# Performance work log

Measured on AMD Instinct MI355X. Metric: run time of the kernel, lower is better.

The kernel has to match this reference:

```python
import jax, jax.numpy as jnp
import numpy as np

B, T, D = 64, 512, 1536   # batch, time, enc_size (2*768)
H = 30                    # z_rnn_size
L_SUP, R_SUP = -0.1, 1.1  # HardKuma stretched support
EPS = 1e-5


def setup_inputs() -> dict:
    key = jax.random.key(0)
    ks = jax.random.split(key, 12)
    s = 0.02
    return {
        "x": jax.random.normal(ks[0], (B, T, D), dtype=jnp.float32),
        "u": jax.random.uniform(ks[1], (B, T, 1), dtype=jnp.float32),
        # LSTMCell(enc_size + 1 -> H), torch gate order [i, f, g, o]
        "Wih": jax.random.normal(ks[2], (4 * H, D + 1), dtype=jnp.float32) * s,
        "Whh": jax.random.normal(ks[3], (4 * H, H), dtype=jnp.float32) * s,
        "bih": jax.random.normal(ks[4], (4 * H,), dtype=jnp.float32) * s,
        "bhh": jax.random.normal(ks[5], (4 * H,), dtype=jnp.float32) * s,
        # KumaGate: Linear(D + H -> 1) + Softplus for a and b
        "Wa": jax.random.normal(ks[6], (1, D + H), dtype=jnp.float32) * s,
        "ba": jax.random.normal(ks[7], (1,), dtype=jnp.float32) * s,
        "Wb": jax.random.normal(ks[8], (1, D + H), dtype=jnp.float32) * s,
        "bb": jax.random.normal(ks[9], (1,), dtype=jnp.float32) * s,
    }


def reference(x, u, Wih, Whh, bih, bhh, Wa, ba, Wb, bb):
    # x: [B, T, D], u: [B, T, 1] uniform reparam noise
    hseq = jnp.swapaxes(x, 0, 1)               # [T, B, D]
    useq = jnp.swapaxes(u, 0, 1)               # [T, B, 1]
    batch = x.shape[0]

    def step(carry, inp):
        hx, cx = carry                          # [B, H] each
        h_t, u_t = inp                          # [B, D], [B, 1]
        feat = jnp.concatenate([h_t, hx], axis=-1)          # [B, D+H]
        a = jnp.clip(jax.nn.softplus(feat @ Wa.T + ba), 1e-6, 100.0)
        b = jnp.clip(jax.nn.softplus(feat @ Wb.T + bb), 1e-6, 100.0)
        # HardKuma reparameterized sample (training branch)
        uu = jnp.clip(u_t, EPS, 1.0 - EPS)
        s = (1.0 - (1.0 - uu) ** (1.0 / b)) ** (1.0 / a)     # Kuma icdf
        t = s * (R_SUP - L_SUP) + L_SUP                      # stretch
        z_t = jnp.clip(t, 0.0, 1.0)                          # hard rectify, [B, 1]
        # LSTMCell update (torch gate order i, f, g, o)
        rnn_in = jnp.concatenate([h_t, z_t], axis=-1)        # [B, D+1]
        gates = rnn_in @ Wih.T + bih + hx @ Whh.T + bhh      # [B, 4H]
        i, f, g, o = jnp.split(gates, 4, axis=-1)
        c_new = jax.nn.sigmoid(f) * cx + jax.nn.sigmoid(i) * jnp.tanh(g)
        h_new = jax.nn.sigmoid(o) * jnp.tanh(c_new)
        return (h_new, c_new), z_t

    init = (jnp.zeros((batch, H), x.dtype), jnp.zeros((batch, H), x.dtype))
    _, zs = jax.lax.scan(step, init, (hseq, useq))           # zs: [T, B, 1]
    return jnp.swapaxes(zs[..., 0], 0, 1)                    # [B, T]
```

## Files before the change

kernel.cpp:

```cpp
#include <hip/hip_runtime.h>
#include <math.h>

#define Bb 64
#define Tt 512
#define Dd 1536
#define Hh 30
#define NC 128
#define Mm (Bb*Tt)
#define KSTEPS 48

typedef unsigned short u16;
typedef __attribute__((ext_vector_type(8))) short short8v;
typedef __attribute__((ext_vector_type(4))) float f32x4;

__device__ __forceinline__ float rcpf_(float x) { return __builtin_amdgcn_rcpf(x); }
__device__ __forceinline__ float sigmoidf_(float x) {
    return rcpf_(1.f + __expf(-x));
}
__device__ __forceinline__ float tanhf_fast(float x) {
    float e = __expf(2.f * x);
    return fmaf(-2.f, rcpf_(e + 1.f), 1.f);
}
__device__ __forceinline__ float softplus_(float x) {
    return fmaxf(x, 0.f) + __logf(1.f + __expf(-fabsf(x)));
}
__device__ __forceinline__ float rl_f(float v, int lane) {
    return __uint_as_float(__builtin_amdgcn_readlane(__float_as_uint(v), lane));
}

#define QPERM(src, CTRL) \
    __uint_as_float((unsigned)__builtin_amdgcn_mov_dpp((int)__float_as_uint(src), CTRL, 0xF, 0xF, false))

#define GLOAD_LDS16(gp, lp) \
    __builtin_amdgcn_global_load_lds((const __attribute__((address_space(1))) void*)(const void*)(gp), \
                                     (__attribute__((address_space(3))) void*)(void*)(lp), 16, 0, 0)

__device__ __forceinline__ f32x4 mm_bf16(short8v a, short8v b, f32x4 c) {
    return __builtin_amdgcn_mfma_f32_16x16x32_bf16(a, b, c, 0, 0, 0);
}

union U4S8 { unsigned int u[4]; short8v s; };

__device__ __forceinline__ void cvt_split(const float4 a, const float4 b,
                                          short8v& hi, short8v& lo) {
    float x[8] = {a.x, a.y, a.z, a.w, b.x, b.y, b.z, b.w};
    U4S8 H, L;
#pragma unroll
    for (int i = 0; i < 4; i++) {
        unsigned int u0 = __float_as_uint(x[2 * i]);
        unsigned int u1 = __float_as_uint(x[2 * i + 1]);
        unsigned int h0 = u0 & 0xffff0000u;
        unsigned int h1 = u1 & 0xffff0000u;
        H.u[i] = (u0 >> 16) | h1;
        float l0 = x[2 * i]     - __uint_as_float(h0);
        float l1 = x[2 * i + 1] - __uint_as_float(h1);
        L.u[i] = (__float_as_uint(l0) >> 16) | (__float_as_uint(l1) & 0xffff0000u);
    }
    hi = H.s;
    lo = L.s;
}

__global__ __launch_bounds__(256) void pack_w(const float* __restrict__ Wih,
                                              const float* __restrict__ Wa,
                                              const float* __restrict__ Wb,
                                              u16* __restrict__ Wbh,
                                              u16* __restrict__ Wbl) {
    const int k = blockIdx.x * 256 + threadIdx.x;
    const int c = blockIdx.y;
    float v = 0.f;
    if (c < 120)       v = Wih[c * (Dd + 1) + k];
    else if (c == 120) v = Wa[k];
    else if (c == 121) v = Wb[k];
    unsigned int u = __float_as_uint(v);
    unsigned int h = u & 0xffff0000u;
    float lo = v - __uint_as_float(h);
    Wbh[(size_t)c * Dd + k] = (u16)(u >> 16);
    Wbl[(size_t)c * Dd + k] = (u16)(__float_as_uint(lo) >> 16);
}

__global__ __launch_bounds__(64) void pack_s3(const float* __restrict__ Wih,
                                              const float* __restrict__ Whh,
                                              const float* __restrict__ Wa,
                                              const float* __restrict__ Wb,
                                              float* __restrict__ WS3) {
    const int l = threadIdx.x;
    const int q = l >> 2, g = l & 3;
    float v0[32], v1[32];
#pragma unroll
    for (int j = 0; j < 32; j++) { v0[j] = 0.f; v1[j] = 0.f; }
    {
        int c0 = g * 30 + q;
        for (int j = 0; j < 30; j++) v0[j] = Whh[c0 * Hh + j];
        v0[30] = Wih[c0 * (Dd + 1) + Dd];
    }
    if (q < 14) {
        int c1 = g * 30 + 16 + q;
        for (int j = 0; j < 30; j++) v1[j] = Whh[c1 * Hh + j];
        v1[30] = Wih[c1 * (Dd + 1) + Dd];
    } else if (l == 56) {
        for (int j = 0; j < 30; j++) v1[j] = Wa[Dd + j];
    } else if (l == 60) {
        for (int j = 0; j < 30; j++) v1[j] = Wb[Dd + j];
    }
    float* dst = WS3 + (size_t)l * 64;
    for (int j = 0; j < 32; j++) { dst[j] = v0[j]; dst[32 + j] = v1[j]; }
}

__global__ __launch_bounds__(256, 2) void gemm_k(const float* __restrict__ X,
                                                 const u16* __restrict__ Wbh,
                                                 const u16* __restrict__ Wbl,
                                                 const float* __restrict__ bih,
                                                 const float* __restrict__ bhh,
                                                 const float* __restrict__ ba,
                                                 const float* __restrict__ bbp,
                                                 float* __restrict__ GX) {
    const int t    = threadIdx.x;
    const int lane = t & 63;
    const int wid  = t >> 6;
    const int wrow = wid >> 1;
    const int wcol = wid & 1;
    const int m0   = blockIdx.x * 64 + wrow * 32;
    const int n0   = wcol * 64;
    const int lr   = lane & 15;
    const int lk   = lane >> 4;

    const float* xa0 = X + (size_t)(m0 + lr) * Dd + lk * 8;
    const float* xa1 = xa0 + (size_t)16 * Dd;
    const u16*   pbh = Wbh + (size_t)(n0 + lr) * Dd + lk * 8;
    const u16*   pbl = Wbl + (size_t)(n0 + lr) * Dd + lk * 8;

    f32x4 acc[2][4];
#pragma unroll
    for (int nt = 0; nt < 4; nt++) {
        int c = n0 + nt * 16 + lr;
        float bv = (c < 120) ? (bih[c] + bhh[c])
                 : (c == 120) ? ba[0]
                 : (c == 121) ? bbp[0] : 0.f;
        f32x4 v = {bv, bv, bv, bv};
        acc[0][nt] = v;
        acc[1][nt] = v;
    }

#define LOADA(ra, ks) do {                                        \
        ra[0] = *(const float4*)(xa0 + (ks) * 32);                \
        ra[1] = *(const float4*)(xa0 + (ks) * 32 + 4);            \
        ra[2] = *(const float4*)(xa1 + (ks) * 32);                \
        ra[3] = *(const float4*)(xa1 + (ks) * 32 + 4);            \
    } while (0)

#define LOADB(bh, bl, ks) do {                                               \
        _Pragma("unroll")                                                    \
        for (int nt = 0; nt < 4; nt++) {                                     \
            bh[nt] = *(const short8v*)(pbh + (size_t)nt * 16 * Dd + (ks) * 32); \
            bl[nt] = *(const short8v*)(pbl + (size_t)nt * 16 * Dd + (ks) * 32); \
        }                                                                    \
    } while (0)

#define STEP(ra, bh, bl) do {                                     \
        short8v ah0, al0, ah1, al1;                               \
        cvt_split(ra[0], ra[1], ah0, al0);                        \
        cvt_split(ra[2], ra[3], ah1, al1);                        \
        _Pragma("unroll")                                         \
        for (int nt = 0; nt < 4; nt++)                            \
            acc[0][nt] = mm_bf16(ah0, bh[nt], acc[0][nt]);        \
        _Pragma("unroll")                                         \
        for (int nt = 0; nt < 4; nt++)                            \
            acc[1][nt] = mm_bf16(ah1, bh[nt], acc[1][nt]);        \
        _Pragma("unroll")                                         \
        for (int nt = 0; nt < 4; nt++)                            \
            acc[0][nt] = mm_bf16(al0, bh[nt], acc[0][nt]);        \
        _Pragma("unroll")                                         \
        for (int nt = 0; nt < 4; nt++)                            \
            acc[1][nt] = mm_bf16(al1, bh[nt], acc[1][nt]);        \
        _Pragma("unroll")                                         \
        for (int nt = 0; nt < 4; nt++)                            \
            acc[0][nt] = mm_bf16(ah0, bl[nt], acc[0][nt]);        \
        _Pragma("unroll")                                         \
        for (int nt = 0; nt < 4; nt++)                            \
            acc[1][nt] = mm_bf16(ah1, bl[nt], acc[1][nt]);        \
    } while (0)

    float4  ra0[4], ra1[4];
    short8v bh0[4], bl0[4], bh1[4], bl1[4];

    LOADA(ra0, 0);
    LOADB(bh0, bl0, 0);
    int ks = 0;
    for (; ks < KSTEPS - 2; ks += 2) {
        LOADA(ra1, ks + 1);
        LOADB(bh1, bl1, ks + 1);
        STEP(ra0, bh0, bl0);
        LOADA(ra0, ks + 2);
        LOADB(bh0, bl0, ks + 2);
        STEP(ra1, bh1, bl1);
    }
    LOADA(ra1, KSTEPS - 1);
    LOADB(bh1, bl1, KSTEPS - 1);
    STEP(ra0, bh0, bl0);
    STEP(ra1, bh1, bl1);

#undef LOADA
#undef LOADB
#undef STEP

#pragma unroll
    for (int mt = 0; mt < 2; mt++)
#pragma unroll
        for (int nt = 0; nt < 4; nt++) {
            float* dst = GX + (size_t)(m0 + mt * 16 + lk * 4) * NC + n0 + nt * 16 + lr;
#pragma unroll
            for (int r = 0; r < 4; r++)
                dst[(size_t)r * NC] = acc[mt][nt][r];
        }
}

#define PIN16(A, B) asm volatile("" \
    : "+v"(A[B+0]), "+v"(A[B+1]), "+v"(A[B+2]),  "+v"(A[B+3]),  "+v"(A[B+4]),  "+v"(A[B+5]),  "+v"(A[B+6]),  "+v"(A[B+7]), \
      "+v"(A[B+8]), "+v"(A[B+9]), "+v"(A[B+10]), "+v"(A[B+11]), "+v"(A[B+12]), "+v"(A[B+13]), "+v"(A[B+14]), "+v"(A[B+15]))

__global__
__attribute__((amdgpu_flat_work_group_size(64, 64)))
__attribute__((amdgpu_waves_per_eu(1)))
void scan_k(const float* __restrict__ u,
            const float* __restrict__ gx,
            const float* __restrict__ WS3,
            float* __restrict__ out) {
    __shared__ float lus[Tt];
    __shared__ float zbuf[Tt];
    __shared__ float gxs[2][32][NC];
    const int b = blockIdx.x;
    const int l = threadIdx.x;
    const int q = l >> 2, g = l & 3;

    for (int k = l; k < Tt; k += 64) {
        float uu = u[b * Tt + k];
        uu = fminf(fmaxf(uu, 1e-5f), 1.f - 1e-5f);
        lus[k] = __logf(1.f - uu);
    }
    __syncthreads();

    float wv0[32], wv1[32];
    {
        const float* wp = WS3 + (size_t)l * 64;
#pragma unroll
        for (int j = 0; j < 8; j++) {
            float4 a4 = ((const float4*)wp)[j];
            float4 b4 = ((const float4*)(wp + 32))[j];
            wv0[4 * j + 0] = a4.x; wv0[4 * j + 1] = a4.y;
            wv0[4 * j + 2] = a4.z; wv0[4 * j + 3] = a4.w;
            wv1[4 * j + 0] = b4.x; wv1[4 * j + 1] = b4.y;
            wv1[4 * j + 2] = b4.z; wv1[4 * j + 3] = b4.w;
        }
    }

    const int c0 = g * 30 + q;
    const int c1 = (q < 14) ? (g * 30 + 16 + q) : ((l == 56) ? 120 : (l == 60) ? 121 : 124);
    const float* gxb0 = gx + (size_t)b * Tt * NC;

    const float mge = (g == 2) ? 2.f : -1.f;

    float hs[Hh];
#pragma unroll
    for (int k = 0; k < Hh; k++) hs[k] = 0.f;
    float cst0 = 0.f, cst1 = 0.f;

#pragma unroll
    for (int j = 0; j < 16; j++)
        GLOAD_LDS16(gxb0 + j * 256 + l * 4, &gxs[0][0][0] + j * 256);
    asm volatile("s_waitcnt vmcnt(0)" ::: "memory");
    float A0 = gxs[0][0][c0], B0 = gxs[0][0][c1], L0 = lus[0];

    for (int c = 0; c < Tt / 32; c++) {
        if (c < Tt / 32 - 1) {
            const float* gch = gxb0 + (size_t)(c + 1) * 32 * NC;
            float* lch = &gxs[(c + 1) & 1][0][0];
#pragma unroll
            for (int j = 0; j < 16; j++)
                GLOAD_LDS16(gch + j * 256 + l * 4, lch + j * 256);
        }
#pragma unroll 1
        for (int s = 0; s < 32; s++) {
            const int t = c * 32 + s;
            PIN16(wv0, 0); PIN16(wv0, 16);
            PIN16(wv1, 0); PIN16(wv1, 16);

            float A1 = 0.f, B1 = 0.f, L1 = 0.f;
            if (t + 1 < Tt) {
                if (s < 31) {
                    A1 = gxs[c & 1][s + 1][c0];
                    B1 = gxs[c & 1][s + 1][c1];
                } else {
                    asm volatile("s_waitcnt vmcnt(0)" ::: "memory");
                    A1 = gxs[(c + 1) & 1][0][c0];
                    B1 = gxs[(c + 1) & 1][0][c1];
                }
                L1 = lus[t + 1];
            }

            float d10 = B0, d11 = 0.f, d12 = 0.f, d13 = 0.f;
#pragma unroll
            for (int k = 0; k < 28; k += 4) {
                d10 = fmaf(wv1[k], hs[k], d10);         d11 = fmaf(wv1[k + 1], hs[k + 1], d11);
                d12 = fmaf(wv1[k + 2], hs[k + 2], d12); d13 = fmaf(wv1[k + 3], hs[k + 3], d13);
            }
            d10 = fmaf(wv1[28], hs[28], d10); d11 = fmaf(wv1[29], hs[29], d11);
            float dot1 = (d10 + d12) + (d11 + d13);

            const float av = rl_f(dot1, 56);
            const float bv = rl_f(dot1, 60);
            float a  = fminf(fmaxf(softplus_(av), 1e-6f), 100.f);
            float bk = fminf(fmaxf(softplus_(bv), 1e-6f), 100.f);
            float lu = L0;
            float p = __expf(lu * rcpf_(bk));
            float inner = 1.f - p;
            float sK = (inner <= 0.f) ? 0.f : __expf(__logf(inner) * rcpf_(a));
            float z = fminf(fmaxf(fmaf(1.2f, sK, -0.1f), 0.f), 1.f);

            float d00 = A0, d01 = 0.f, d02 = 0.f, d03 = 0.f;
#pragma unroll
            for (int k = 0; k < 28; k += 4) {
                d00 = fmaf(wv0[k], hs[k], d00);         d01 = fmaf(wv0[k + 1], hs[k + 1], d01);
                d02 = fmaf(wv0[k + 2], hs[k + 2], d02); d03 = fmaf(wv0[k + 3], hs[k + 3], d03);
            }
            d00 = fmaf(wv0[28], hs[28], d00); d01 = fmaf(wv0[29], hs[29], d01);
            float dot0 = (d00 + d02) + (d01 + d03);

            float acc0 = fmaf(z, wv0[30], dot0);
            float acc1 = fmaf(z, wv1[30], dot1);

            float e0 = __expf(acc0 * mge);
            float e1 = __expf(acc1 * mge);
            float r0 = rcpf_(1.f + e0);
            float r1 = rcpf_(1.f + e1);
            float val0 = (g == 2) ? fmaf(-2.f, r0, 1.f) : r0;
            float val1 = (g == 2) ? fmaf(-2.f, r1, 1.f) : r1;

            float vf0 = QPERM(val0, 0x55), vg0 = QPERM(val0, 0xAA), vo0 = QPERM(val0, 0xFF);
            float vf1 = QPERM(val1, 0x55), vg1 = QPERM(val1, 0xAA), vo1 = QPERM(val1, 0xFF);

            float cn0 = fmaf(vf0, cst0, val0 * vg0);
            float hn0 = vo0 * tanhf_fast(cn0);
            cst0 = cn0;
            float cn1 = fmaf(vf1, cst1, val1 * vg1);
            float hn1 = vo1 * tanhf_fast(cn1);
            cst1 = cn1;

#pragma unroll
            for (int k = 0; k < 16; k++) hs[k] = rl_f(hn0, 4 * k);
#pragma unroll
            for (int k = 16; k < Hh; k++) hs[k] = rl_f(hn1, 4 * (k - 16));

            if (l == 0) zbuf[t] = z;
            A0 = A1; B0 = B1; L0 = L1;
        }
    }
    __syncthreads();
    for (int k = l; k < Tt; k += 64) out[b * Tt + k] = zbuf[k];
}

extern "C" void kernel_launch(void* const* d_in, const int* in_sizes, int n_in,
                              void* d_out, int out_size, void* d_ws, size_t ws_size,
                              hipStream_t stream) {
    const float* x   = (const float*)d_in[0];
    const float* u   = (const float*)d_in[1];
    const float* Wih = (const float*)d_in[2];
    const float* Whh = (const float*)d_in[3];
    const float* bih = (const float*)d_in[4];
    const float* bhh = (const float*)d_in[5];
    const float* Wa  = (const float*)d_in[6];
    const float* ba  = (const float*)d_in[7];
    const float* Wb  = (const float*)d_in[8];
    const float* bbp = (const float*)d_in[9];
    float* out = (float*)d_out;

    char* wsb = (char*)d_ws;
    u16*   Wbh = (u16*)(wsb);
    u16*   Wbl = (u16*)(wsb + 393216);
    float* WS3 = (float*)(wsb + 786432);
    float* GX  = (float*)(wsb + 802816);

    pack_w<<<dim3(Dd / 256, NC), 256, 0, stream>>>(Wih, Wa, Wb, Wbh, Wbl);
    pack_s3<<<1, 64, 0, stream>>>(Wih, Whh, Wa, Wb, WS3);
    gemm_k<<<Mm / 64, 256, 0, stream>>>(x, Wbh, Wbl, bih, bhh, ba, bbp, GX);
    scan_k<<<Bb, 64, 0, stream>>>(u, GX, WS3, out);
}
```

Before: 649.5 us.

## Fuse pack, GEMM and scan into one cooperative kernel with grid syncs

Merges the weight packing, input-projection GEMM and recurrent scan into a single cooperative megakernel of 256 blocks, separated by grid-wide syncs, to remove three kernel-launch boundaries. Each block now does two GEMM tiles, and the scan runs with 256-thread blocks where only 64 threads work. The cost is a serialised scan phase that still sits on 64 blocks, lower occupancy in the GEMM phase (launch bounds 256,1), and grid-sync overhead. The old separate kernels remain as a fallback if the cooperative launch fails.

```diff
diff --git a/kernel.cpp b/kernel.cpp
--- a/kernel.cpp
+++ b/kernel.cpp
@@ -1,5 +1,8 @@
 #include <hip/hip_runtime.h>
+#include <hip/hip_cooperative_groups.h>
 #include <math.h>
+
+namespace cg = cooperative_groups;
 
 #define Bb 64
 #define Tt 512
@@ -60,30 +63,38 @@
     lo = L.s;
 }
 
-__global__ __launch_bounds__(256) void pack_w(const float* __restrict__ Wih,
-                                              const float* __restrict__ Wa,
-                                              const float* __restrict__ Wb,
-                                              u16* __restrict__ Wbh,
-                                              u16* __restrict__ Wbl) {
-    const int k = blockIdx.x * 256 + threadIdx.x;
-    const int c = blockIdx.y;
-    float v = 0.f;
-    if (c < 120)       v = Wih[c * (Dd + 1) + k];
-    else if (c == 120) v = Wa[k];
-    else if (c == 121) v = Wb[k];
-    unsigned int u = __float_as_uint(v);
-    unsigned int h = u & 0xffff0000u;
-    float lo = v - __uint_as_float(h);
-    Wbh[(size_t)c * Dd + k] = (u16)(u >> 16);
-    Wbl[(size_t)c * Dd + k] = (u16)(__float_as_uint(lo) >> 16);
-}
-
-__global__ __launch_bounds__(64) void pack_s3(const float* __restrict__ Wih,
-                                              const float* __restrict__ Whh,
-                                              const float* __restrict__ Wa,
-                                              const float* __restrict__ Wb,
-                                              float* __restrict__ WS3) {
-    const int l = threadIdx.x;
+#define PIN16(A, B) asm volatile("" \
+    : "+v"(A[B+0]), "+v"(A[B+1]), "+v"(A[B+2]),  "+v"(A[B+3]),  "+v"(A[B+4]),  "+v"(A[B+5]),  "+v"(A[B+6]),  "+v"(A[B+7]), \
+      "+v"(A[B+8]), "+v"(A[B+9]), "+v"(A[B+10]), "+v"(A[B+11]), "+v"(A[B+12]), "+v"(A[B+13]), "+v"(A[B+14]), "+v"(A[B+15]))
+
+
+__device__ __forceinline__ void pack_w_body(int i0, int stride,
+                                            const float* __restrict__ Wih,
+                                            const float* __restrict__ Wa,
+                                            const float* __restrict__ Wb,
+                                            u16* __restrict__ Wbh,
+                                            u16* __restrict__ Wbl) {
+    for (int i = i0; i < NC * Dd; i += stride) {
+        int c = i / Dd;
+        int k = i - c * Dd;
+        float v = 0.f;
+        if (c < 120)       v = Wih[c * (Dd + 1) + k];
+        else if (c == 120) v = Wa[k];
+        else if (c == 121) v = Wb[k];
+        unsigned int u = __float_as_uint(v);
+        unsigned int h = u & 0xffff0000u;
+        float lo = v - __uint_as_float(h);
+        Wbh[i] = (u16)(u >> 16);
+        Wbl[i] = (u16)(__float_as_uint(lo) >> 16);
+    }
+}
+
+__device__ __forceinline__ void pack_s3_body(int l,
+                                             const float* __restrict__ Wih,
+                                             const float* __restrict__ Whh,
+                                             const float* __restrict__ Wa,
+                                             const float* __restrict__ Wb,
+                                             float* __restrict__ WS3) {
     const int q = l >> 2, g = l & 3;
     float v0[32], v1[32];
 #pragma unroll
@@ -106,20 +117,20 @@
     for (int j = 0; j < 32; j++) { dst[j] = v0[j]; dst[32 + j] = v1[j]; }
 }
 
-__global__ __launch_bounds__(256, 2) void gemm_k(const float* __restrict__ X,
-                                                 const u16* __restrict__ Wbh,
-                                                 const u16* __restrict__ Wbl,
-                                                 const float* __restrict__ bih,
-                                                 const float* __restrict__ bhh,
-                                                 const float* __restrict__ ba,
-                                                 const float* __restrict__ bbp,
-                                                 float* __restrict__ GX) {
-    const int t    = threadIdx.x;
+__device__ void gemm_tile(int tileIdx, int t,
+                          const float* __restrict__ X,
+                          const u16* __restrict__ Wbh,
+                          const u16* __restrict__ Wbl,
+                          const float* __restrict__ bih,
+                          const float* __restrict__ bhh,
+                          const float* __restrict__ ba,
+                          const float* __restrict__ bbp,
+                          float* __restrict__ GX) {
     const int lane = t & 63;
     const int wid  = t >> 6;
     const int wrow = wid >> 1;
     const int wcol = wid & 1;
-    const int m0   = blockIdx.x * 64 + wrow * 32;
+    const int m0   = tileIdx * 64 + wrow * 32;
     const int n0   = wcol * 64;
     const int lr   = lane & 15;
     const int lk   = lane >> 4;
@@ -214,148 +225,207 @@
         }
 }
 
-#define PIN16(A, B) asm volatile("" \
-    : "+v"(A[B+0]), "+v"(A[B+1]), "+v"(A[B+2]),  "+v"(A[B+3]),  "+v"(A[B+4]),  "+v"(A[B+5]),  "+v"(A[B+6]),  "+v"(A[B+7]), \
-      "+v"(A[B+8]), "+v"(A[B+9]), "+v"(A[B+10]), "+v"(A[B+11]), "+v"(A[B+12]), "+v"(A[B+13]), "+v"(A[B+14]), "+v"(A[B+15]))
-
-__global__
-__attribute__((amdgpu_flat_work_group_size(64, 64)))
-__attribute__((amdgpu_waves_per_eu(1)))
-void scan_k(const float* __restrict__ u,
-            const float* __restrict__ gx,
-            const float* __restrict__ WS3,
-            float* __restrict__ out) {
+__device__ void scan_body(int b, int tid,
+                          const float* __restrict__ u,
+                          const float* __restrict__ gx,
+                          const float* __restrict__ WS3,
+                          float* __restrict__ out) {
     __shared__ float lus[Tt];
     __shared__ float zbuf[Tt];
     __shared__ float gxs[2][32][NC];
-    const int b = blockIdx.x;
-    const int l = threadIdx.x;
-    const int q = l >> 2, g = l & 3;
-
-    for (int k = l; k < Tt; k += 64) {
-        float uu = u[b * Tt + k];
-        uu = fminf(fmaxf(uu, 1e-5f), 1.f - 1e-5f);
-        lus[k] = __logf(1.f - uu);
+    const int l = tid;
+
+    if (l < 64) {
+        for (int k = l; k < Tt; k += 64) {
+            float uu = u[b * Tt + k];
+            uu = fminf(fmaxf(uu, 1e-5f), 1.f - 1e-5f);
+            lus[k] = __logf(1.f - uu);
+        }
     }
     __syncthreads();
 
-    float wv0[32], wv1[32];
-    {
-        const float* wp = WS3 + (size_t)l * 64;
-#pragma unroll
-        for (int j = 0; j < 8; j++) {
-            float4 a4 = ((const float4*)wp)[j];
-            float4 b4 = ((const float4*)(wp + 32))[j];
-            wv0[4 * j + 0] = a4.x; wv0[4 * j + 1] = a4.y;
-            wv0[4 * j + 2] = a4.z; wv0[4 * j + 3] = a4.w;
-            wv1[4 * j + 0] = b4.x; wv1[4 * j + 1] = b4.y;
-            wv1[4 * j + 2] = b4.z; wv1[4 * j + 3] = b4.w;
+    if (l < 64) {
+        const int q = l >> 2, g = l & 3;
+
+        float wv0[32], wv1[32];
+        {
+            const float* wp = WS3 + (size_t)l * 64;
+#pragma unroll
+            for (int j = 0; j < 8; j++) {
+                float4 a4 = ((const float4*)wp)[j];
+                float4 b4 = ((const float4*)(wp + 32))[j];
+                wv0[4 * j + 0] = a4.x; wv0[4 * j + 1] = a4.y;
+                wv0[4 * j + 2] = a4.z; wv0[4 * j + 3] = a4.w;
+                wv1[4 * j + 0] = b4.x; wv1[4 * j + 1] = b4.y;
+                wv1[4 * j + 2] = b4.z; wv1[4 * j + 3] = b4.w;
+            }
         }
-    }
-
-    const int c0 = g * 30 + q;
-    const int c1 = (q < 14) ? (g * 30 + 16 + q) : ((l == 56) ? 120 : (l == 60) ? 121 : 124);
-    const float* gxb0 = gx + (size_t)b * Tt * NC;
-
-    const float mge = (g == 2) ? 2.f : -1.f;
-
-    float hs[Hh];
-#pragma unroll
-    for (int k = 0; k < Hh; k++) hs[k] = 0.f;
-    float cst0 = 0.f, cst1 = 0.f;
-
-#pragma unroll
-    for (int j = 0; j < 16; j++)
-        GLOAD_LDS16(gxb0 + j * 256 + l * 4, &gxs[0][0][0] + j * 256);
-    asm volatile("s_waitcnt vmcnt(0)" ::: "memory");
-    float A0 = gxs[0][0][c0], B0 = gxs[0][0][c1], L0 = lus[0];
-
-    for (int c = 0; c < Tt / 32; c++) {
-        if (c < Tt / 32 - 1) {
-            const float* gch = gxb0 + (size_t)(c + 1) * 32 * NC;
-            float* lch = &gxs[(c + 1) & 1][0][0];
-#pragma unroll
-            for (int j = 0; j < 16; j++)
-                GLOAD_LDS16(gch + j * 256 + l * 4, lch + j * 256);
+
+        const int c0 = g * 30 + q;
+        const int c1 = (q < 14) ? (g * 30 + 16 + q) : ((l == 56) ? 120 : (l == 60) ? 121 : 124);
+        const float* gxb0 = gx + (size_t)b * Tt * NC;
+        const float mge = (g == 2) ? 2.f : -1.f;
+
+        float hs[Hh];
+#pragma unroll
+        for (int k = 0; k < Hh; k++) hs[k] = 0.f;
+        float cst0 = 0.f, cst1 = 0.f;
+
+#pragma unroll
+        for (int j = 0; j < 16; j++)
+            GLOAD_LDS16(gxb0 + j * 256 + l * 4, &gxs[0][0][0] + j * 256);
+        asm volatile("s_waitcnt vmcnt(0)" ::: "memory");
+        float A0 = gxs[0][0][c0], B0 = gxs[0][0][c1], L0 = lus[0];
+
+        for (int c = 0; c < Tt / 32; c++) {
+            if (c < Tt / 32 - 1) {
+                const float* gch = gxb0 + (size_t)(c + 1) * 32 * NC;
+                float* lch = &gxs[(c + 1) & 1][0][0];
+#pragma unroll
+                for (int j = 0; j < 16; j++)
+                    GLOAD_LDS16(gch + j * 256 + l * 4, lch + j * 256);
+            }
+#pragma unroll 1
+            for (int s = 0; s < 32; s++) {
+                const int t = c * 32 + s;
+                PIN16(wv0, 0); PIN16(wv0, 16);
+                PIN16(wv1, 0); PIN16(wv1, 16);
+
+                float A1 = 0.f, B1 = 0.f, L1 = 0.f;
+                if (t + 1 < Tt) {
+                    if (s < 31) {
+                        A1 = gxs[c & 1][s + 1][c0];
+                        B1 = gxs[c & 1][s + 1][c1];
+                    } else {
+                        asm volatile("s_waitcnt vmcnt(0)" ::: "memory");
+                        A1 = gxs[(c + 1) & 1][0][c0];
+                        B1 = gxs[(c + 1) & 1][0][c1];
+                    }
+                    L1 = lus[t + 1];
+                }
+
+                float d10 = B0, d11 = 0.f, d12 = 0.f, d13 = 0.f;
+#pragma unroll
+                for (int k = 0; k < 28; k += 4) {
+                    d10 = fmaf(wv1[k], hs[k], d10);         d11 = fmaf(wv1[k + 1], hs[k + 1], d11);
+                    d12 = fmaf(wv1[k + 2], hs[k + 2], d12); d13 = fmaf(wv1[k + 3], hs[k + 3], d13);
+                }
+                d10 = fmaf(wv1[28], hs[28], d10); d11 = fmaf(wv1[29], hs[29], d11);
+                float dot1 = (d10 + d12) + (d11 + d13);
+
+                const float av = rl_f(dot1, 56);
+                const float bv = rl_f(dot1, 60);
+                float a  = fminf(fmaxf(softplus_(av), 1e-6f), 100.f);
+                float bk = fminf(fmaxf(softplus_(bv), 1e-6f), 100.f);
+                float lu = L0;
+                float p = __expf(lu * rcpf_(bk));
+                float inner = 1.f - p;
+                float sK = (inner <= 0.f) ? 0.f : __expf(__logf(inner) * rcpf_(a));
+                float z = fminf(fmaxf(fmaf(1.2f, sK, -0.1f), 0.f), 1.f);
+
+                float d00 = A0, d01 = 0.f, d02 = 0.f, d03 = 0.f;
+#pragma unroll
+                for (int k = 0; k < 28; k += 4) {
+                    d00 = fmaf(wv0[k], hs[k], d00);         d01 = fmaf(wv0[k + 1], hs[k + 1], d01);
+                    d02 = fmaf(wv0[k + 2], hs[k + 2], d02); d03 = fmaf(wv0[k + 3], hs[k + 3], d03);
+                }
+                d00 = fmaf(wv0[28], hs[28], d00); d01 = fmaf(wv0[29], hs[29], d01);
+                float dot0 = (d00 + d02) + (d01 + d03);
+
+                float acc0 = fmaf(z, wv0[30], dot0);
+                float acc1 = fmaf(z, wv1[30], dot1);
+
+                float e0 = __expf(acc0 * mge);
+                float e1 = __expf(acc1 * mge);
+                float r0 = rcpf_(1.f + e0);
+                float r1 = rcpf_(1.f + e1);
+                float val0 = (g == 2) ? fmaf(-2.f, r0, 1.f) : r0;
+                float val1 = (g == 2) ? fmaf(-2.f, r1, 1.f) : r1;
+
+                float vf0 = QPERM(val0, 0x55), vg0 = QPERM(val0, 0xAA), vo0 = QPERM(val0, 0xFF);
+                float vf1 = QPERM(val1, 0x55), vg1 = QPERM(val1, 0xAA), vo1 = QPERM(val1, 0xFF);
+
+                float cn0 = fmaf(vf0, cst0, val0 * vg0);
+                float hn0 = vo0 * tanhf_fast(cn0);
+                cst0 = cn0;
+                float cn1 = fmaf(vf1, cst1, val1 * vg1);
+                float hn1 = vo1 * tanhf_fast(cn1);
+                cst1 = cn1;
+
+#pragma unroll
+                for (int k = 0; k < 16; k++) hs[k] = rl_f(hn0, 4 * k);
+#pragma unroll
+                for (int k = 16; k < Hh; k++) hs[k] = rl_f(hn1, 4 * (k - 16));
+
+                if (l == 0) zbuf[t] = z;
+                A0 = A1; B0 = B1; L0 = L1;
+            }
         }
-#pragma unroll 1
-        for (int s = 0; s < 32; s++) {
-            const int t = c * 32 + s;
-            PIN16(wv0, 0); PIN16(wv0, 16);
-            PIN16(wv1, 0); PIN16(wv1, 16);
-
-            float A1 = 0.f, B1 = 0.f, L1 = 0.f;
-            if (t + 1 < Tt) {
-                if (s < 31) {
-                    A1 = gxs[c & 1][s + 1][c0];
-                    B1 = gxs[c & 1][s + 1][c1];
-                } else {
-                    asm volatile("s_waitcnt vmcnt(0)" ::: "memory");
-                    A1 = gxs[(c + 1) & 1][0][c0];
-                    B1 = gxs[(c + 1) & 1][0][c1];
-                }
-                L1 = lus[t + 1];
-            }
-
-            float d10 = B0, d11 = 0.f, d12 = 0.f, d13 = 0.f;
-#pragma unroll
-            for (int k = 0; k < 28; k += 4) {
-                d10 = fmaf(wv1[k], hs[k], d10);         d11 = fmaf(wv1[k + 1], hs[k + 1], d11);
-                d12 = fmaf(wv1[k + 2], hs[k + 2], d12); d13 = fmaf(wv1[k + 3], hs[k + 3], d13);
-            }
-            d10 = fmaf(wv1[28], hs[28], d10); d11 = fmaf(wv1[29], hs[29], d11);
-            float dot1 = (d10 + d12) + (d11 + d13);
-
-            const float av = rl_f(dot1, 56);
-            const float bv = rl_f(dot1, 60);
-            float a  = fminf(fmaxf(softplus_(av), 1e-6f), 100.f);
-            float bk = fminf(fmaxf(softplus_(bv), 1e-6f), 100.f);
-            float lu = L0;
-            float p = __expf(lu * rcpf_(bk));
-            float inner = 1.f - p;
-            float sK = (inner <= 0.f) ? 0.f : __expf(__logf(inner) * rcpf_(a));
-            float z = fminf(fmaxf(fmaf(1.2f, sK, -0.1f), 0.f), 1.f);
-
-            float d00 = A0, d01 = 0.f, d02 = 0.f, d03 = 0.f;
-#pragma unroll
-            for (int k = 0; k < 28; k += 4) {
-                d00 = fmaf(wv0[k], hs[k], d00);         d01 = fmaf(wv0[k + 1], hs[k + 1], d01);
-                d02 = fmaf(wv0[k + 2], hs[k + 2], d02); d03 = fmaf(wv0[k + 3], hs[k + 3], d03);
-            }
-            d00 = fmaf(wv0[28], hs[28], d00); d01 = fmaf(wv0[29], hs[29], d01);
-            float dot0 = (d00 + d02) + (d01 + d03);
-
-            float acc0 = fmaf(z, wv0[30], dot0);
-            float acc1 = fmaf(z, wv1[30], dot1);
-
-            float e0 = __expf(acc0 * mge);
-            float e1 = __expf(acc1 * mge);
-            float r0 = rcpf_(1.f + e0);
-            float r1 = rcpf_(1.f + e1);
-            float val0 = (g == 2) ? fmaf(-2.f, r0, 1.f) : r0;
-            float val1 = (g == 2) ? fmaf(-2.f, r1, 1.f) : r1;
-
-            float vf0 = QPERM(val0, 0x55), vg0 = QPERM(val0, 0xAA), vo0 = QPERM(val0, 0xFF);
-            float vf1 = QPERM(val1, 0x55), vg1 = QPERM(val1, 0xAA), vo1 = QPERM(val1, 0xFF);
-
-            float cn0 = fmaf(vf0, cst0, val0 * vg0);
-            float hn0 = vo0 * tanhf_fast(cn0);
-            cst0 = cn0;
-            float cn1 = fmaf(vf1, cst1, val1 * vg1);
-            float hn1 = vo1 * tanhf_fast(cn1);
-            cst1 = cn1;
-
-#pragma unroll
-            for (int k = 0; k < 16; k++) hs[k] = rl_f(hn0, 4 * k);
-#pragma unroll
-            for (int k = 16; k < Hh; k++) hs[k] = rl_f(hn1, 4 * (k - 16));
-
-            if (l == 0) zbuf[t] = z;
-            A0 = A1; B0 = B1; L0 = L1;
-        }
     }
     __syncthreads();
-    for (int k = l; k < Tt; k += 64) out[b * Tt + k] = zbuf[k];
+    if (l < 64) {
+        for (int k = l; k < Tt; k += 64) out[b * Tt + k] = zbuf[k];
+    }
+}
+
+__global__ __launch_bounds__(256, 1)
+void mega_k(const float* __restrict__ x, const float* __restrict__ u,
+            const float* __restrict__ Wih, const float* __restrict__ Whh,
+            const float* __restrict__ bih, const float* __restrict__ bhh,
+            const float* __restrict__ Wa, const float* __restrict__ ba,
+            const float* __restrict__ Wb, const float* __restrict__ bbp,
+            u16* __restrict__ Wbh, u16* __restrict__ Wbl,
+            float* __restrict__ WS3, float* __restrict__ GX,
+            float* __restrict__ out) {
+    const int blk = blockIdx.x;
+    const int tid = threadIdx.x;
+
+    pack_w_body(blk * 256 + tid, 256 * 256, Wih, Wa, Wb, Wbh, Wbl);
+    if (blk == 0 && tid < 64) pack_s3_body(tid, Wih, Whh, Wa, Wb, WS3);
+    __threadfence();
+    cg::this_grid().sync();
+
+    gemm_tile(blk * 2 + 0, tid, x, Wbh, Wbl, bih, bhh, ba, bbp, GX);
+    gemm_tile(blk * 2 + 1, tid, x, Wbh, Wbl, bih, bhh, ba, bbp, GX);
+    __threadfence();
+    cg::this_grid().sync();
+
+    if (blk >= 64) return;
+    scan_body(blk, tid, u, GX, WS3, out);
+}
+
+__global__ __launch_bounds__(256) void pack_w_k(const float* __restrict__ Wih,
+                                                const float* __restrict__ Wa,
+                                                const float* __restrict__ Wb,
+                                                u16* __restrict__ Wbh,
+                                                u16* __restrict__ Wbl) {
+    pack_w_body(blockIdx.x * 256 + threadIdx.x, gridDim.x * 256, Wih, Wa, Wb, Wbh, Wbl);
+}
+
+__global__ __launch_bounds__(64) void pack_s3_k(const float* __restrict__ Wih,
+                                                const float* __restrict__ Whh,
+                                                const float* __restrict__ Wa,
+                                                const float* __restrict__ Wb,
+                                                float* __restrict__ WS3) {
+    pack_s3_body(threadIdx.x, Wih, Whh, Wa, Wb, WS3);
+}
+
+__global__ __launch_bounds__(256, 2) void gemm_k(const float* __restrict__ X,
+                                                 const u16* __restrict__ Wbh,
+                                                 const u16* __restrict__ Wbl,
+                                                 const float* __restrict__ bih,
+                                                 const float* __restrict__ bhh,
+                                                 const float* __restrict__ ba,
+                                                 const float* __restrict__ bbp,
+                                                 float* __restrict__ GX) {
+    gemm_tile(blockIdx.x, threadIdx.x, X, Wbh, Wbl, bih, bhh, ba, bbp, GX);
+}
+
+__global__ __launch_bounds__(256, 1) void scan_k(const float* __restrict__ u,
+                                                 const float* __restrict__ gx,
+                                                 const float* __restrict__ WS3,
+                                                 float* __restrict__ out) {
+    scan_body(blockIdx.x, threadIdx.x, u, gx, WS3, out);
 }
 
 extern "C" void kernel_launch(void* const* d_in, const int* in_sizes, int n_in,
@@ -379,8 +449,17 @@
     float* WS3 = (float*)(wsb + 786432);
     float* GX  = (float*)(wsb + 802816);
 
-    pack_w<<<dim3(Dd / 256, NC), 256, 0, stream>>>(Wih, Wa, Wb, Wbh, Wbl);
-    pack_s3<<<1, 64, 0, stream>>>(Wih, Whh, Wa, Wb, WS3);
-    gemm_k<<<Mm / 64, 256, 0, stream>>>(x, Wbh, Wbl, bih, bhh, ba, bbp, GX);
-    scan_k<<<Bb, 64, 0, stream>>>(u, GX, WS3, out);
-}
+    void* args[] = {
+        (void*)&x, (void*)&u, (void*)&Wih, (void*)&Whh, (void*)&bih, (void*)&bhh,
+        (void*)&Wa, (void*)&ba, (void*)&Wb, (void*)&bbp,
+        (void*)&Wbh, (void*)&Wbl, (void*)&WS3, (void*)&GX, (void*)&out
+    };
+    hipError_t e = hipLaunchCooperativeKernel((const void*)mega_k, dim3(256), dim3(256),
+                                              args, 0, stream);
+    if (e != hipSuccess) {
+        pack_w_k<<<(Dd * NC) / 256 / 4, 256, 0, stream>>>(Wih, Wa, Wb, Wbh, Wbl);
+        pack_s3_k<<<1, 64, 0, stream>>>(Wih, Whh, Wa, Wb, WS3);
+        gemm_k<<<Mm / 64, 256, 0, stream>>>(x, Wbh, Wbl, bih, bhh, ba, bbp, GX);
+        scan_k<<<Bb, 256, 0, stream>>>(u, GX, WS3, out);
+    }
+}
```

After: 771.1 us. 18.7% more time.
